# Kernel tuning notes

Hardware: AMD Instinct MI355X
Metric: run time of the kernel (lower is better)

The kernel has to match this reference:

```python
import jax, jax.numpy as jnp
import numpy as np

NUM_GROUPS = 32
EPS = 1e-5

def setup_inputs() -> dict:
    key = jax.random.key(0)
    ks = jax.random.split(key, 10)
    N, C, H, W = 4, 128, 64, 64
    x = jax.random.normal(ks[0], (N, C, H, W), dtype=jnp.float32)
    # GroupNorm affine params
    gn_scale = jnp.ones((C,), dtype=jnp.float32)
    gn_bias = jnp.zeros((C,), dtype=jnp.float32)
    # 1x1 conv weights [out, in] (xavier_uniform scale)
    lim = float(np.sqrt(6.0 / (C + C)))
    wq = jax.random.uniform(ks[1], (C, C), minval=-lim, maxval=lim, dtype=jnp.float32)
    wk = jax.random.uniform(ks[2], (C, C), minval=-lim, maxval=lim, dtype=jnp.float32)
    wv = jax.random.uniform(ks[3], (C, C), minval=-lim, maxval=lim, dtype=jnp.float32)
    wp = jax.random.uniform(ks[4], (C, C), minval=-lim, maxval=lim, dtype=jnp.float32) * 1e-5
    bq = jnp.zeros((C,), dtype=jnp.float32)
    bk = jnp.zeros((C,), dtype=jnp.float32)
    bv = jnp.zeros((C,), dtype=jnp.float32)
    bp = jnp.zeros((C,), dtype=jnp.float32)
    return {"x": x, "gn_scale": gn_scale, "gn_bias": gn_bias,
            "wq": wq, "bq": bq, "wk": wk, "bk": bk,
            "wv": wv, "bv": bv, "wp": wp, "bp": bp}

def _group_norm(x, scale, bias):
    # x: [N, C, H, W]
    N, C, H, W = x.shape
    g = x.reshape(N, NUM_GROUPS, C // NUM_GROUPS, H, W)
    mean = g.mean(axis=(2, 3, 4), keepdims=True)
    var = g.var(axis=(2, 3, 4), keepdims=True)
    g = (g - mean) * jax.lax.rsqrt(var + EPS)
    x = g.reshape(N, C, H, W)
    return x * scale[None, :, None, None] + bias[None, :, None, None]

def reference(x, gn_scale, gn_bias, wq, bq, wk, bk, wv, bv, wp, bp):
    N, C, H, W = x.shape
    h = _group_norm(x, gn_scale, gn_bias)
    # flatten spatial to tokens: [N, HW, C]
    ht = h.reshape(N, C, H * W).transpose(0, 2, 1)
    q = jnp.einsum('nlc,oc->nlo', ht, wq) + bq
    k = jnp.einsum('nlc,oc->nlo', ht, wk) + bk
    v = jnp.einsum('nlc,oc->nlo', ht, wv) + bv
    score = jnp.einsum('nqc,nkc->nqk', q, k) * (C ** -0.5)  # [N, HW, HW]
    attn = jax.nn.softmax(score, axis=-1)
    out = jnp.einsum('nqk,nkc->nqc', attn, v)  # [N, HW, C]
    out = jnp.einsum('nlc,oc->nlo', out, wp) + bp
    out = out.transpose(0, 2, 1).reshape(N, C, H, W)
    return x + out
```

## Files before the change

kernel.cpp:

```cpp
#include <hip/hip_runtime.h>

#define HW 4096
#define CCH 128
#define NB 4

typedef short bf16x8 __attribute__((ext_vector_type(8)));
typedef float f32x4 __attribute__((ext_vector_type(4)));

__device__ __forceinline__ unsigned short f2bf(float f){
  union { float fv; unsigned u; } v; v.fv = f;
  unsigned r = v.u + 0x7fffu + ((v.u >> 16) & 1u);
  return (unsigned short)(r >> 16);
}
__device__ __forceinline__ float bf2f(unsigned short u){
  return __uint_as_float(((unsigned)u) << 16);
}
__device__ __forceinline__ f32x4 mfma16(bf16x8 a, bf16x8 b, f32x4 c){
  return __builtin_amdgcn_mfma_f32_16x16x32_bf16(a, b, c, 0, 0, 0);
}
__device__ __forceinline__ void gll16(const void* g, void* l){
  __builtin_amdgcn_global_load_lds(
      (const __attribute__((address_space(1))) unsigned*)g,
      (__attribute__((address_space(3))) unsigned*)l, 16, 0, 0);
}

__global__ __launch_bounds__(256) void gn_stats_k(const float* __restrict__ x,
    float* __restrict__ stats,
    const float* __restrict__ wq, const float* __restrict__ wk,
    const float* __restrict__ wv, const float* __restrict__ wp,
    unsigned short* __restrict__ wqb, unsigned short* __restrict__ wkb,
    unsigned short* __restrict__ wvb, unsigned short* __restrict__ wpb){
  int tid = threadIdx.x;
  if (tid < 128){
    int f4 = blockIdx.x * 128 + tid;
    int m = f4 >> 12, e = f4 & 4095;
    const float* s4 = (m == 0) ? wq : ((m == 1) ? wk : ((m == 2) ? wv : wp));
    unsigned short* d4 = (m == 0) ? wqb : ((m == 1) ? wkb : ((m == 2) ? wvb : wpb));
    float4 v = *(const float4*)(s4 + e * 4);
    ushort4 b; b.x = f2bf(v.x); b.y = f2bf(v.y); b.z = f2bf(v.z); b.w = f2bf(v.w);
    *(ushort4*)(d4 + e * 4) = b;
  }
  int gid = blockIdx.x;
  const float4* p = (const float4*)(x + (size_t)gid * 16384);
  float s = 0.f, q = 0.f;
  #pragma unroll
  for (int i = 0; i < 16; i++){
    float4 v = p[tid + 256 * i];
    s += v.x + v.y + v.z + v.w;
    q += v.x * v.x + v.y * v.y + v.z * v.z + v.w * v.w;
  }
  #pragma unroll
  for (int d = 1; d < 64; d <<= 1){ s += __shfl_xor(s, d); q += __shfl_xor(q, d); }
  __shared__ float red[8];
  int w = tid >> 6;
  if ((tid & 63) == 0){ red[2 * w] = s; red[2 * w + 1] = q; }
  __syncthreads();
  if (tid == 0){
    float S = red[0] + red[2] + red[4] + red[6];
    float Q = red[1] + red[3] + red[5] + red[7];
    float mean = S * (1.f / 16384.f);
    float var  = Q * (1.f / 16384.f) - mean * mean;
    stats[2 * gid]     = mean;
    stats[2 * gid + 1] = rsqrtf(var + 1e-5f);
  }
}

__global__ __launch_bounds__(256) void gn_apply_k(const float* __restrict__ x,
    const float* __restrict__ stats, const float* __restrict__ sc,
    const float* __restrict__ bi, unsigned short* __restrict__ ht){
  int n = blockIdx.y, l0 = blockIdx.x * 32, tid = threadIdx.x;
  __shared__ __align__(16) unsigned short hs[32][136];
  #pragma unroll
  for (int i = 0; i < 16; i++){
    int c = (tid >> 5) + 8 * i;
    int l = tid & 31;
    float v = x[((size_t)(n * CCH + c)) * HW + l0 + l];
    int grp = n * 32 + (c >> 2);
    float r = (v - stats[2 * grp]) * stats[2 * grp + 1] * sc[c] + bi[c];
    hs[l][c] = f2bf(r);
  }
  __syncthreads();
  #pragma unroll
  for (int i = 0; i < 2; i++){
    int ch = tid + 256 * i;
    int l = ch >> 4, cb = (ch & 15) * 8;
    *(uint4*)&ht[((size_t)(n * HW) + l0 + l) * CCH + cb] = *(const uint4*)&hs[l][cb];
  }
}

__global__ __launch_bounds__(256, 3) void qkv_k(const unsigned short* __restrict__ ht,
    const unsigned short* __restrict__ wqb, const unsigned short* __restrict__ wkb,
    const unsigned short* __restrict__ wvb,
    const float* __restrict__ bq, const float* __restrict__ bk,
    const float* __restrict__ bv,
    unsigned short* __restrict__ Qg, unsigned short* __restrict__ Kg,
    unsigned short* __restrict__ Vt){
  int n = blockIdx.y, l0 = blockIdx.x * 64, m = blockIdx.z, tid = threadIdx.x;
  int w = tid >> 6, lane = tid & 63, l15 = lane & 15, g = lane >> 4;
  __shared__ __align__(16) char lds[49152];
  char* hA = lds;
  char* WB = lds + 16384;
  const unsigned short* wsrc = (m == 0) ? wqb : ((m == 1) ? wkb : wvb);
  const float* bsrc = (m == 0) ? bq : ((m == 1) ? bk : bv);
  {
    const char* hb = (const char*)ht + ((size_t)(n * HW) + l0) * (CCH * 2);
    #pragma unroll
    for (int i = 0; i < 4; i++){
      int T = (4 * w + i) * 64 + lane;
      int row = T >> 4, c16 = (T & 15) ^ (row & 15);
      gll16(hb + row * 256 + c16 * 16, hA + (4 * w + i) * 1024);
    }
    const char* wb2 = (const char*)wsrc;
    #pragma unroll
    for (int i = 0; i < 8; i++){
      int T = (8 * w + i) * 64 + lane;
      int row = T >> 4, c16 = (T & 15) ^ (row & 15);
      gll16(wb2 + row * 256 + c16 * 16, WB + (8 * w + i) * 1024);
    }
  }
  __syncthreads();
  bf16x8 a[4];
  #pragma unroll
  for (int kc = 0; kc < 4; kc++)
    a[kc] = *(const bf16x8*)(hA + (16 * w + l15) * 256 + ((4 * kc + g) ^ l15) * 16);
  f32x4 acc[8];
  #pragma unroll
  for (int ct = 0; ct < 8; ct++) acc[ct] = (f32x4)(0.f);
  #pragma unroll
  for (int ct = 0; ct < 8; ct++)
    #pragma unroll
    for (int kc = 0; kc < 4; kc++){
      bf16x8 bfr = *(const bf16x8*)(WB + (16 * ct + l15) * 256 + ((4 * kc + g) ^ l15) * 16);
      acc[ct] = mfma16(a[kc], bfr, acc[ct]);
    }
  __syncthreads();
  if (m < 2){
    float qs = (m == 0) ? 0.08838834764831845f : 1.0f;
    unsigned short* dst = (m == 0) ? Qg : Kg;
    unsigned short* os = (unsigned short*)(lds + 16384);
    #pragma unroll
    for (int ct = 0; ct < 8; ct++){
      int o = 16 * ct + l15;
      float bias = bsrc[o];
      #pragma unroll
      for (int r = 0; r < 4; r++)
        os[(16 * w + 4 * g + r) * 136 + o] = f2bf((acc[ct][r] + bias) * qs);
    }
    __syncthreads();
    #pragma unroll
    for (int i = 0; i < 4; i++){
      int T = tid + 256 * i;
      int row = T >> 4, cb = T & 15;
      *(uint4*)&dst[((size_t)(n * HW) + l0 + row) * CCH + cb * 8] =
          *(const uint4*)&os[row * 136 + cb * 8];
    }
  } else {
    unsigned short* os = (unsigned short*)(lds + 16384);
    #pragma unroll
    for (int ct = 0; ct < 8; ct++){
      int o = 16 * ct + l15;
      float bias = bsrc[o];
      #pragma unroll
      for (int r = 0; r < 4; r++)
        os[o * 72 + 16 * w + 4 * g + r] = f2bf(acc[ct][r] + bias);
    }
    __syncthreads();
    #pragma unroll
    for (int i = 0; i < 4; i++){
      int T = tid + 256 * i;
      int row = T >> 3, c = T & 7;
      *(uint4*)&Vt[((size_t)(n * CCH) + row) * HW + l0 + c * 8] =
          *(const uint4*)&os[row * 72 + c * 8];
    }
  }
}

__global__ __launch_bounds__(256, 4) void attn_k(const unsigned short* __restrict__ Qg,
    const unsigned short* __restrict__ Kg, const unsigned short* __restrict__ Vt,
    unsigned short* __restrict__ Op, float* __restrict__ Ml, int lsp){
  int nbk = gridDim.x, cpx = nbk >> 3, b = blockIdx.x;
  int swz = (b & 7) * cpx + (b >> 3);
  int q0 = (swz & 63) * 64;
  int rest = swz >> 6;
  int splits = 1 << lsp;
  int sp = rest & (splits - 1);
  int n = rest >> lsp;
  int kvs = HW >> lsp, nt = 64 >> lsp;
  int tid = threadIdx.x;
  int w = tid >> 6, lane = tid & 63, l15 = lane & 15, g = lane >> 4;
  __shared__ __align__(16) char lds[32768];
  char* Ks = lds;
  char* Vs = lds + 16384;

  bf16x8 qf[4];
  #pragma unroll
  for (int kc = 0; kc < 4; kc++)
    qf[kc] = *reinterpret_cast<const bf16x8*>(
        &Qg[((size_t)(n * HW) + q0 + 16 * w + l15) * CCH + 32 * kc + 8 * g]);
  f32x4 ov[8];
  #pragma unroll
  for (int i = 0; i < 8; i++) ov[i] = (f32x4)(0.f);
  float mrun = -3.0e38f, lrun = 0.f;

  const char* kp[4]; const char* vp[4];
  {
    const char* kbase = (const char*)Kg + ((size_t)(n * HW) + sp * kvs) * (CCH * 2);
    const char* vbase = (const char*)Vt + (size_t)(n * CCH) * (HW * 2) + (size_t)sp * kvs * 2;
    #pragma unroll
    for (int i = 0; i < 4; i++){
      int C = (w * 4 + i) * 64 + lane;
      int row = C >> 4, c16 = (C & 15) ^ (row & 15);
      kp[i] = kbase + row * 256 + c16 * 16;
      int vrow = C >> 3, c8 = (C & 7) ^ (vrow & 7);
      vp[i] = vbase + (size_t)vrow * (HW * 2) + c8 * 16;
    }
  }
  char* kl = Ks + w * 4096;
  char* vl = Vs + w * 4096;

  for (int t = 0; t < nt; t++){
    __syncthreads();
    #pragma unroll
    for (int i = 0; i < 4; i++) gll16(kp[i] + (size_t)t * 16384, kl + i * 1024);
    #pragma unroll
    for (int i = 0; i < 4; i++) gll16(vp[i] + (size_t)t * 128,   vl + i * 1024);
    __syncthreads();

    f32x4 s[4];
    __builtin_amdgcn_s_setprio(1);
    #pragma unroll
    for (int ct = 0; ct < 4; ct++){
      f32x4 acc = (f32x4)(0.f);
      #pragma unroll
      for (int kc = 0; kc < 4; kc++){
        bf16x8 kf = *(const bf16x8*)(Ks + (16 * ct + l15) * 256 + ((4 * kc + g) ^ l15) * 16);
        acc = mfma16(kf, qf[kc], acc);
      }
      s[ct] = acc;
    }
    __builtin_amdgcn_s_setprio(0);

    float mx = -3.0e38f;
    #pragma unroll
    for (int ct = 0; ct < 4; ct++)
      #pragma unroll
      for (int r = 0; r < 4; r++) mx = fmaxf(mx, s[ct][r]);
    mx = fmaxf(mx, __shfl_xor(mx, 16));
    mx = fmaxf(mx, __shfl_xor(mx, 32));
    if (__any(mx > mrun + 8.0f)){
      float mn = fmaxf(mrun, mx);
      float al = __expf(mrun - mn);
      mrun = mn; lrun *= al;
      #pragma unroll
      for (int ct = 0; ct < 8; ct++)
        #pragma unroll
        for (int r = 0; r < 4; r++) ov[ct][r] *= al;
    }
    float rs = 0.f;
    #pragma unroll
    for (int ct = 0; ct < 4; ct++)
      #pragma unroll
      for (int r = 0; r < 4; r++){
        float e = __expf(s[ct][r] - mrun);
        s[ct][r] = e;
        rs += e;
      }
    rs += __shfl_xor(rs, 16);
    rs += __shfl_xor(rs, 32);
    lrun += rs;

    unsigned up[4][2];
    #pragma unroll
    for (int ct = 0; ct < 4; ct++)
      #pragma unroll
      for (int h = 0; h < 2; h++)
        up[ct][h] = (unsigned)f2bf(s[ct][2 * h]) |
                    ((unsigned)f2bf(s[ct][2 * h + 1]) << 16);
    union { unsigned u[2][4]; bf16x8 v[2]; } pb;
    #pragma unroll
    for (int kc = 0; kc < 2; kc++)
      #pragma unroll
      for (int j = 0; j < 4; j++){
        int src = (((j + ((g & 1) << 2)) >> 1) << 4) + l15;
        unsigned v0 = (unsigned)__shfl((int)up[2 * kc][j & 1], src);
        unsigned v1 = (unsigned)__shfl((int)up[2 * kc + 1][j & 1], src);
        pb.u[kc][j] = (g & 2) ? v1 : v0;
      }

    __builtin_amdgcn_s_setprio(1);
    #pragma unroll
    for (int ct = 0; ct < 8; ct++){
      #pragma unroll
      for (int kc = 0; kc < 2; kc++){
        bf16x8 vf = *(const bf16x8*)(Vs + (16 * ct + l15) * 128 + ((4 * kc + g) ^ (l15 & 7)) * 16);
        ov[ct] = mfma16(vf, pb.v[kc], ov[ct]);
      }
    }
    __builtin_amdgcn_s_setprio(0);
  }
  float inv = 1.f / lrun;
  (void)inv;
  size_t obase = (size_t)((sp * NB + n) * HW);
  size_t qrow = obase + q0 + 16 * w + l15;
  #pragma unroll
  for (int ct = 0; ct < 8; ct++){
    ushort4 pk;
    pk.x = f2bf(ov[ct][0]); pk.y = f2bf(ov[ct][1]);
    pk.z = f2bf(ov[ct][2]); pk.w = f2bf(ov[ct][3]);
    *(ushort4*)&Op[qrow * CCH + 16 * ct + 4 * g] = pk;
  }
  if (g == 0){
    Ml[qrow * 2]     = mrun;
    Ml[qrow * 2 + 1] = lrun;
  }
}

__global__ __launch_bounds__(256) void projout_k(const unsigned short* __restrict__ Op,
    const float* __restrict__ Ml, const unsigned short* __restrict__ wpb,
    const float* __restrict__ bp, const float* __restrict__ x,
    float* __restrict__ out, int splits){
  int n = blockIdx.y, l0 = blockIdx.x * 32, tid = threadIdx.x;
  int w = tid >> 6, lane = tid & 63, l15 = lane & 15, g = lane >> 4;
  __shared__ __align__(16) unsigned short hs[32][136];
  __shared__ __align__(16) char WB[32768];
  {
    const char* wb2 = (const char*)wpb;
    #pragma unroll
    for (int i = 0; i < 8; i++){
      int T = (8 * w + i) * 64 + lane;
      int row = T >> 4, c16 = (T & 15) ^ (row & 15);
      gll16(wb2 + row * 256 + c16 * 16, WB + (8 * w + i) * 1024);
    }
  }
  const size_t SSTR = (size_t)NB * HW;
  #pragma unroll
  for (int i = 0; i < 2; i++){
    int T = tid + 256 * i;
    int row = T >> 4, cb = (T & 15) * 8;
    size_t gl = (size_t)n * HW + l0 + row;
    float mv = -3.0e38f;
    #pragma unroll
    for (int s = 0; s < 4; s++)
      if (s < splits) mv = fmaxf(mv, Ml[(s * SSTR + gl) * 2]);
    float fa[8];
    #pragma unroll
    for (int j = 0; j < 8; j++) fa[j] = 0.f;
    float denom = 0.f;
    #pragma unroll
    for (int s = 0; s < 4; s++){
      if (s < splits){
        float wgt = __expf(Ml[(s * SSTR + gl) * 2] - mv);
        denom += wgt * Ml[(s * SSTR + gl) * 2 + 1];
        uint4 a = *(const uint4*)&Op[(s * SSTR + gl) * CCH + cb];
        const unsigned short* au = (const unsigned short*)&a;
        #pragma unroll
        for (int j = 0; j < 8; j++) fa[j] += wgt * bf2f(au[j]);
      }
    }
    float inv = 1.f / denom;
    #pragma unroll
    for (int j = 0; j < 8; j++) hs[row][cb + j] = f2bf(fa[j] * inv);
  }
  __syncthreads();
  int rt = w & 1, cg = w >> 1;
  bf16x8 a[4];
  #pragma unroll
  for (int kc = 0; kc < 4; kc++)
    a[kc] = *reinterpret_cast<const bf16x8*>(&hs[16 * rt + l15][32 * kc + 8 * g]);
  f32x4 acc[4];
  #pragma unroll
  for (int ci = 0; ci < 4; ci++) acc[ci] = (f32x4)(0.f);
  #pragma unroll
  for (int ci = 0; ci < 4; ci++){
    int o = 16 * (cg * 4 + ci) + l15;
    #pragma unroll
    for (int kc = 0; kc < 4; kc++){
      bf16x8 bfr = *(const bf16x8*)(WB + o * 256 + ((4 * kc + g) ^ l15) * 16);
      acc[ci] = mfma16(a[kc], bfr, acc[ci]);
    }
  }
  #pragma unroll
  for (int ci = 0; ci < 4; ci++){
    int o = 16 * (cg * 4 + ci) + l15;
    float bias = bp[o];
    size_t base = ((size_t)(n * CCH) + o) * HW + l0 + 16 * rt + 4 * g;
    float4 xr = *(const float4*)&x[base];
    float4 res;
    res.x = xr.x + acc[ci][0] + bias;
    res.y = xr.y + acc[ci][1] + bias;
    res.z = xr.z + acc[ci][2] + bias;
    res.w = xr.w + acc[ci][3] + bias;
    *(float4*)&out[base] = res;
  }
}

extern "C" void kernel_launch(void* const* d_in, const int* in_sizes, int n_in,
                              void* d_out, int out_size, void* d_ws, size_t ws_size,
                              hipStream_t stream){
  const float* x    = (const float*)d_in[0];
  const float* gnsc = (const float*)d_in[1];
  const float* gnb  = (const float*)d_in[2];
  const float* wq   = (const float*)d_in[3];
  const float* bq   = (const float*)d_in[4];
  const float* wk   = (const float*)d_in[5];
  const float* bk   = (const float*)d_in[6];
  const float* wv   = (const float*)d_in[7];
  const float* bv   = (const float*)d_in[8];
  const float* wp   = (const float*)d_in[9];
  const float* bp   = (const float*)d_in[10];
  float* out = (float*)d_out;

  char* ws = (char*)d_ws;
  const size_t BUF = (size_t)NB * HW * CCH * sizeof(unsigned short);
  const size_t WOFF = 4096;
  const size_t HTOFF = WOFF + 4 * 32768;
  const size_t NEED4 = HTOFF + 8 * BUF + (size_t)4 * NB * HW * 2 * sizeof(float);
  const int lsp = (ws_size >= NEED4) ? 2 : 1;
  const int splits = 1 << lsp;

  float* stats        = (float*)ws;
  unsigned short* wqb = (unsigned short*)(ws + WOFF);
  unsigned short* wkb = (unsigned short*)(ws + WOFF + 32768);
  unsigned short* wvb = (unsigned short*)(ws + WOFF + 65536);
  unsigned short* wpb = (unsigned short*)(ws + WOFF + 98304);
  unsigned short* ht  = (unsigned short*)(ws + HTOFF);
  unsigned short* Qg  = (unsigned short*)(ws + HTOFF + BUF);
  unsigned short* Kg  = (unsigned short*)(ws + HTOFF + 2 * BUF);
  unsigned short* Vt  = (unsigned short*)(ws + HTOFF + 3 * BUF);
  unsigned short* Op  = (unsigned short*)(ws + HTOFF + 4 * BUF);
  float*          Ml  = (float*)(ws + HTOFF + 4 * BUF + (size_t)splits * BUF);

  gn_stats_k<<<128, 256, 0, stream>>>(x, stats, wq, wk, wv, wp, wqb, wkb, wvb, wpb);
  gn_apply_k<<<dim3(128, NB), 256, 0, stream>>>(x, stats, gnsc, gnb, ht);
  qkv_k<<<dim3(64, NB, 3), 256, 0, stream>>>(ht, wqb, wkb, wvb, bq, bk, bv, Qg, Kg, Vt);
  attn_k<<<dim3(64 * NB * splits), 256, 0, stream>>>(Qg, Kg, Vt, Op, Ml, lsp);
  projout_k<<<dim3(128, NB), 256, 0, stream>>>(Op, Ml, wpb, bp, x, out, splits);
}
```

Before: 157.6 us.

## Fuse GroupNorm apply into QKV kernel and double-buffer attention KV tiles

The separate GroupNorm-apply kernel is folded into the QKV projection kernel. Each block now normalizes fp32 x directly into a swizzled bf16 LDS tile, which removes the ht intermediate buffer and one kernel launch. The attention kernel switches to 32-key tiles held in two LDS buffers, issuing the next tile's async loads before computing on the current one so memory latency overlaps the MFMA work. The costs are more loop iterations, each with a barrier, smaller MFMA batches per iteration, and a redundant reread of x across the three q/k/v blocks.

Measured after the change: 159.9 us. About the same (+1.4%).

```diff
diff --git a/kernel.cpp b/kernel.cpp
--- a/kernel.cpp
+++ b/kernel.cpp
@@ -65,30 +65,9 @@
   }
 }
 
-__global__ __launch_bounds__(256) void gn_apply_k(const float* __restrict__ x,
+__global__ __launch_bounds__(256, 3) void gnqkv_k(const float* __restrict__ x,
     const float* __restrict__ stats, const float* __restrict__ sc,
-    const float* __restrict__ bi, unsigned short* __restrict__ ht){
-  int n = blockIdx.y, l0 = blockIdx.x * 32, tid = threadIdx.x;
-  __shared__ __align__(16) unsigned short hs[32][136];
-  #pragma unroll
-  for (int i = 0; i < 16; i++){
-    int c = (tid >> 5) + 8 * i;
-    int l = tid & 31;
-    float v = x[((size_t)(n * CCH + c)) * HW + l0 + l];
-    int grp = n * 32 + (c >> 2);
-    float r = (v - stats[2 * grp]) * stats[2 * grp + 1] * sc[c] + bi[c];
-    hs[l][c] = f2bf(r);
-  }
-  __syncthreads();
-  #pragma unroll
-  for (int i = 0; i < 2; i++){
-    int ch = tid + 256 * i;
-    int l = ch >> 4, cb = (ch & 15) * 8;
-    *(uint4*)&ht[((size_t)(n * HW) + l0 + l) * CCH + cb] = *(const uint4*)&hs[l][cb];
-  }
-}
-
-__global__ __launch_bounds__(256, 3) void qkv_k(const unsigned short* __restrict__ ht,
+    const float* __restrict__ bi,
     const unsigned short* __restrict__ wqb, const unsigned short* __restrict__ wkb,
     const unsigned short* __restrict__ wvb,
     const float* __restrict__ bq, const float* __restrict__ bk,
@@ -103,19 +82,33 @@
   const unsigned short* wsrc = (m == 0) ? wqb : ((m == 1) ? wkb : wvb);
   const float* bsrc = (m == 0) ? bq : ((m == 1) ? bk : bv);
   {
-    const char* hb = (const char*)ht + ((size_t)(n * HW) + l0) * (CCH * 2);
-    #pragma unroll
-    for (int i = 0; i < 4; i++){
-      int T = (4 * w + i) * 64 + lane;
-      int row = T >> 4, c16 = (T & 15) ^ (row & 15);
-      gll16(hb + row * 256 + c16 * 16, hA + (4 * w + i) * 1024);
-    }
     const char* wb2 = (const char*)wsrc;
     #pragma unroll
     for (int i = 0; i < 8; i++){
       int T = (8 * w + i) * 64 + lane;
       int row = T >> 4, c16 = (T & 15) ^ (row & 15);
       gll16(wb2 + row * 256 + c16 * 16, WB + (8 * w + i) * 1024);
+    }
+  }
+  #pragma unroll
+  for (int i = 0; i < 8; i++){
+    int F = tid + 256 * i;
+    int c = F >> 4, l4 = F & 15;
+    float4 v = *(const float4*)&x[((size_t)(n * CCH + c)) * HW + l0 + l4 * 4];
+    int grp = n * 32 + (c >> 2);
+    float mean = stats[2 * grp], rstd = stats[2 * grp + 1];
+    float scl = rstd * sc[c];
+    float off = bi[c] - mean * scl;
+    float r0 = v.x * scl + off, r1 = v.y * scl + off;
+    float r2 = v.z * scl + off, r3 = v.w * scl + off;
+    int slotbase = ((c >> 3) << 4) ^ 0;
+    (void)slotbase;
+    #pragma unroll
+    for (int j = 0; j < 4; j++){
+      int l = l4 * 4 + j;
+      float rv = (j == 0) ? r0 : ((j == 1) ? r1 : ((j == 2) ? r2 : r3));
+      int slot = (c >> 3) ^ (l & 15);
+      *(unsigned short*)(hA + l * 256 + slot * 16 + ((c & 7) << 1)) = f2bf(rv);
     }
   }
   __syncthreads();
@@ -185,12 +178,11 @@
   int splits = 1 << lsp;
   int sp = rest & (splits - 1);
   int n = rest >> lsp;
-  int kvs = HW >> lsp, nt = 64 >> lsp;
+  int kvs = HW >> lsp;
+  int nt = kvs >> 5;
   int tid = threadIdx.x;
   int w = tid >> 6, lane = tid & 63, l15 = lane & 15, g = lane >> 4;
   __shared__ __align__(16) char lds[32768];
-  char* Ks = lds;
-  char* Vs = lds + 16384;
 
   bf16x8 qf[4];
   #pragma unroll
@@ -202,49 +194,55 @@
   for (int i = 0; i < 8; i++) ov[i] = (f32x4)(0.f);
   float mrun = -3.0e38f, lrun = 0.f;
 
-  const char* kp[4]; const char* vp[4];
+  const char* kp[2]; const char* vp[2];
   {
     const char* kbase = (const char*)Kg + ((size_t)(n * HW) + sp * kvs) * (CCH * 2);
     const char* vbase = (const char*)Vt + (size_t)(n * CCH) * (HW * 2) + (size_t)sp * kvs * 2;
     #pragma unroll
-    for (int i = 0; i < 4; i++){
-      int C = (w * 4 + i) * 64 + lane;
-      int row = C >> 4, c16 = (C & 15) ^ (row & 15);
-      kp[i] = kbase + row * 256 + c16 * 16;
-      int vrow = C >> 3, c8 = (C & 7) ^ (vrow & 7);
-      vp[i] = vbase + (size_t)vrow * (HW * 2) + c8 * 16;
-    }
-  }
-  char* kl = Ks + w * 4096;
-  char* vl = Vs + w * 4096;
+    for (int i = 0; i < 2; i++){
+      int C = (w * 2 + i) * 64 + lane;
+      int kr = C >> 4, ks = (C & 15) ^ (kr & 15);
+      kp[i] = kbase + kr * 256 + ks * 16;
+      int vr = C >> 2, vsl = (C & 3) ^ ((vr >> 1) & 3);
+      vp[i] = vbase + (size_t)vr * (HW * 2) + vsl * 16;
+    }
+  }
+
+  #pragma unroll
+  for (int i = 0; i < 2; i++){
+    gll16(kp[i], lds + w * 2048 + i * 1024);
+    gll16(vp[i], lds + 8192 + w * 2048 + i * 1024);
+  }
+  __syncthreads();
 
   for (int t = 0; t < nt; t++){
-    __syncthreads();
-    #pragma unroll
-    for (int i = 0; i < 4; i++) gll16(kp[i] + (size_t)t * 16384, kl + i * 1024);
-    #pragma unroll
-    for (int i = 0; i < 4; i++) gll16(vp[i] + (size_t)t * 128,   vl + i * 1024);
-    __syncthreads();
-
-    f32x4 s[4];
+    char* cur = lds + ((t & 1) << 14);
+    if (t + 1 < nt){
+      char* nb = lds + (((t + 1) & 1) << 14);
+      #pragma unroll
+      for (int i = 0; i < 2; i++){
+        gll16(kp[i] + (size_t)(t + 1) * 8192, nb + w * 2048 + i * 1024);
+        gll16(vp[i] + (size_t)(t + 1) * 64,   nb + 8192 + w * 2048 + i * 1024);
+      }
+    }
+    char* Ks = cur; char* Vs = cur + 8192;
+
+    f32x4 s[2];
     __builtin_amdgcn_s_setprio(1);
     #pragma unroll
-    for (int ct = 0; ct < 4; ct++){
+    for (int ct = 0; ct < 2; ct++){
       f32x4 acc = (f32x4)(0.f);
       #pragma unroll
       for (int kc = 0; kc < 4; kc++){
-        bf16x8 kf = *(const bf16x8*)(Ks + (16 * ct + l15) * 256 + ((4 * kc + g) ^ l15) * 16);
+        bf16x8 kf = *(const bf16x8*)(Ks + (16 * ct + l15) * 256 + (((4 * kc + g) ^ l15) << 4));
         acc = mfma16(kf, qf[kc], acc);
       }
       s[ct] = acc;
     }
     __builtin_amdgcn_s_setprio(0);
 
-    float mx = -3.0e38f;
-    #pragma unroll
-    for (int ct = 0; ct < 4; ct++)
-      #pragma unroll
-      for (int r = 0; r < 4; r++) mx = fmaxf(mx, s[ct][r]);
+    float mx = fmaxf(fmaxf(fmaxf(s[0][0], s[0][1]), fmaxf(s[0][2], s[0][3])),
+                     fmaxf(fmaxf(s[1][0], s[1][1]), fmaxf(s[1][2], s[1][3])));
     mx = fmaxf(mx, __shfl_xor(mx, 16));
     mx = fmaxf(mx, __shfl_xor(mx, 32));
     if (__any(mx > mrun + 8.0f)){
@@ -258,7 +256,7 @@
     }
     float rs = 0.f;
     #pragma unroll
-    for (int ct = 0; ct < 4; ct++)
+    for (int ct = 0; ct < 2; ct++)
       #pragma unroll
       for (int r = 0; r < 4; r++){
         float e = __expf(s[ct][r] - mrun);
@@ -269,37 +267,32 @@
     rs += __shfl_xor(rs, 32);
     lrun += rs;
 
-    unsigned up[4][2];
-    #pragma unroll
-    for (int ct = 0; ct < 4; ct++)
+    unsigned up[2][2];
+    #pragma unroll
+    for (int ct = 0; ct < 2; ct++)
       #pragma unroll
       for (int h = 0; h < 2; h++)
         up[ct][h] = (unsigned)f2bf(s[ct][2 * h]) |
                     ((unsigned)f2bf(s[ct][2 * h + 1]) << 16);
-    union { unsigned u[2][4]; bf16x8 v[2]; } pb;
-    #pragma unroll
-    for (int kc = 0; kc < 2; kc++)
-      #pragma unroll
-      for (int j = 0; j < 4; j++){
-        int src = (((j + ((g & 1) << 2)) >> 1) << 4) + l15;
-        unsigned v0 = (unsigned)__shfl((int)up[2 * kc][j & 1], src);
-        unsigned v1 = (unsigned)__shfl((int)up[2 * kc + 1][j & 1], src);
-        pb.u[kc][j] = (g & 2) ? v1 : v0;
-      }
+    union { unsigned u[4]; bf16x8 v; } pb;
+    #pragma unroll
+    for (int j = 0; j < 4; j++){
+      int src = (((((g & 1) << 2) + j) >> 1) << 4) + l15;
+      unsigned v0 = (unsigned)__shfl((int)up[0][j & 1], src);
+      unsigned v1 = (unsigned)__shfl((int)up[1][j & 1], src);
+      pb.u[j] = (g & 2) ? v1 : v0;
+    }
 
     __builtin_amdgcn_s_setprio(1);
     #pragma unroll
     for (int ct = 0; ct < 8; ct++){
-      #pragma unroll
-      for (int kc = 0; kc < 2; kc++){
-        bf16x8 vf = *(const bf16x8*)(Vs + (16 * ct + l15) * 128 + ((4 * kc + g) ^ (l15 & 7)) * 16);
-        ov[ct] = mfma16(vf, pb.v[kc], ov[ct]);
-      }
+      int row = 16 * ct + l15;
+      bf16x8 vf = *(const bf16x8*)(Vs + row * 64 + ((g ^ ((row >> 1) & 3)) << 4));
+      ov[ct] = mfma16(vf, pb.v, ov[ct]);
     }
     __builtin_amdgcn_s_setprio(0);
-  }
-  float inv = 1.f / lrun;
-  (void)inv;
+    __syncthreads();
+  }
   size_t obase = (size_t)((sp * NB + n) * HW);
   size_t qrow = obase + q0 + 16 * w + l15;
   #pragma unroll
@@ -413,8 +406,8 @@
   char* ws = (char*)d_ws;
   const size_t BUF = (size_t)NB * HW * CCH * sizeof(unsigned short);
   const size_t WOFF = 4096;
-  const size_t HTOFF = WOFF + 4 * 32768;
-  const size_t NEED4 = HTOFF + 8 * BUF + (size_t)4 * NB * HW * 2 * sizeof(float);
+  const size_t QOFF = WOFF + 4 * 32768;
+  const size_t NEED4 = QOFF + 7 * BUF + (size_t)4 * NB * HW * 2 * sizeof(float);
   const int lsp = (ws_size >= NEED4) ? 2 : 1;
   const int splits = 1 << lsp;
 
@@ -423,16 +416,15 @@
   unsigned short* wkb = (unsigned short*)(ws + WOFF + 32768);
   unsigned short* wvb = (unsigned short*)(ws + WOFF + 65536);
   unsigned short* wpb = (unsigned short*)(ws + WOFF + 98304);
-  unsigned short* ht  = (unsigned short*)(ws + HTOFF);
-  unsigned short* Qg  = (unsigned short*)(ws + HTOFF + BUF);
-  unsigned short* Kg  = (unsigned short*)(ws + HTOFF + 2 * BUF);
-  unsigned short* Vt  = (unsigned short*)(ws + HTOFF + 3 * BUF);
-  unsigned short* Op  = (unsigned short*)(ws + HTOFF + 4 * BUF);
-  float*          Ml  = (float*)(ws + HTOFF + 4 * BUF + (size_t)splits * BUF);
+  unsigned short* Qg  = (unsigned short*)(ws + QOFF);
+  unsigned short* Kg  = (unsigned short*)(ws + QOFF + BUF);
+  unsigned short* Vt  = (unsigned short*)(ws + QOFF + 2 * BUF);
+  unsigned short* Op  = (unsigned short*)(ws + QOFF + 3 * BUF);
+  float*          Ml  = (float*)(ws + QOFF + 3 * BUF + (size_t)splits * BUF);
 
   gn_stats_k<<<128, 256, 0, stream>>>(x, stats, wq, wk, wv, wp, wqb, wkb, wvb, wpb);
-  gn_apply_k<<<dim3(128, NB), 256, 0, stream>>>(x, stats, gnsc, gnb, ht);
-  qkv_k<<<dim3(64, NB, 3), 256, 0, stream>>>(ht, wqb, wkb, wvb, bq, bk, bv, Qg, Kg, Vt);
+  gnqkv_k<<<dim3(64, NB, 3), 256, 0, stream>>>(x, stats, gnsc, gnb,
+      wqb, wkb, wvb, bq, bk, bv, Qg, Kg, Vt);
   attn_k<<<dim3(64 * NB * splits), 256, 0, stream>>>(Qg, Kg, Vt, Op, Ml, lsp);
   projout_k<<<dim3(128, NB), 256, 0, stream>>>(Op, Ml, wpb, bp, x, out, splits);
 }
```

## Fuse GroupNorm apply into QKV projection and use exp2 softmax with more splits

Applied to the files above, without the earlier changes.

Removes the separate gn_apply kernel and its bf16 ht buffer. Each QKV block now normalizes its own x tile and writes it in swizzled form into LDS. The log2(e) factor is folded into the Q scale so that attention and the split combine use exp2f instead of __expf. It also allows up to 8 KV splits when the workspace is large enough and raises attn occupancy to 5 blocks. In exchange, x is re-read and re-normalized three times, once per Q/K/V block, and the 8-way split adds more partial-output traffic in the combine step.

New measurement: 174.2 us. +10.5%, slower.

```diff
diff --git a/kernel.cpp b/kernel.cpp
--- a/kernel.cpp
+++ b/kernel.cpp
@@ -65,30 +65,9 @@
   }
 }
 
-__global__ __launch_bounds__(256) void gn_apply_k(const float* __restrict__ x,
+__global__ __launch_bounds__(256, 3) void gnqkv_k(const float* __restrict__ x,
     const float* __restrict__ stats, const float* __restrict__ sc,
-    const float* __restrict__ bi, unsigned short* __restrict__ ht){
-  int n = blockIdx.y, l0 = blockIdx.x * 32, tid = threadIdx.x;
-  __shared__ __align__(16) unsigned short hs[32][136];
-  #pragma unroll
-  for (int i = 0; i < 16; i++){
-    int c = (tid >> 5) + 8 * i;
-    int l = tid & 31;
-    float v = x[((size_t)(n * CCH + c)) * HW + l0 + l];
-    int grp = n * 32 + (c >> 2);
-    float r = (v - stats[2 * grp]) * stats[2 * grp + 1] * sc[c] + bi[c];
-    hs[l][c] = f2bf(r);
-  }
-  __syncthreads();
-  #pragma unroll
-  for (int i = 0; i < 2; i++){
-    int ch = tid + 256 * i;
-    int l = ch >> 4, cb = (ch & 15) * 8;
-    *(uint4*)&ht[((size_t)(n * HW) + l0 + l) * CCH + cb] = *(const uint4*)&hs[l][cb];
-  }
-}
-
-__global__ __launch_bounds__(256, 3) void qkv_k(const unsigned short* __restrict__ ht,
+    const float* __restrict__ bi,
     const unsigned short* __restrict__ wqb, const unsigned short* __restrict__ wkb,
     const unsigned short* __restrict__ wvb,
     const float* __restrict__ bq, const float* __restrict__ bk,
@@ -103,13 +82,6 @@
   const unsigned short* wsrc = (m == 0) ? wqb : ((m == 1) ? wkb : wvb);
   const float* bsrc = (m == 0) ? bq : ((m == 1) ? bk : bv);
   {
-    const char* hb = (const char*)ht + ((size_t)(n * HW) + l0) * (CCH * 2);
-    #pragma unroll
-    for (int i = 0; i < 4; i++){
-      int T = (4 * w + i) * 64 + lane;
-      int row = T >> 4, c16 = (T & 15) ^ (row & 15);
-      gll16(hb + row * 256 + c16 * 16, hA + (4 * w + i) * 1024);
-    }
     const char* wb2 = (const char*)wsrc;
     #pragma unroll
     for (int i = 0; i < 8; i++){
@@ -118,6 +90,25 @@
       gll16(wb2 + row * 256 + c16 * 16, WB + (8 * w + i) * 1024);
     }
   }
+  #pragma unroll
+  for (int i = 0; i < 8; i++){
+    int F = tid + 256 * i;
+    int c = F >> 4, l4 = F & 15;
+    float4 v = *(const float4*)&x[((size_t)(n * CCH + c)) * HW + l0 + l4 * 4];
+    int grp = n * 32 + (c >> 2);
+    float mean = stats[2 * grp], rstd = stats[2 * grp + 1];
+    float scl = rstd * sc[c];
+    float off = bi[c] - mean * scl;
+    float r0 = v.x * scl + off, r1 = v.y * scl + off;
+    float r2 = v.z * scl + off, r3 = v.w * scl + off;
+    #pragma unroll
+    for (int j = 0; j < 4; j++){
+      int l = l4 * 4 + j;
+      float rv = (j == 0) ? r0 : ((j == 1) ? r1 : ((j == 2) ? r2 : r3));
+      int slot = (c >> 3) ^ (l & 15);
+      *(unsigned short*)(hA + l * 256 + slot * 16 + ((c & 7) << 1)) = f2bf(rv);
+    }
+  }
   __syncthreads();
   bf16x8 a[4];
   #pragma unroll
@@ -135,7 +126,7 @@
     }
   __syncthreads();
   if (m < 2){
-    float qs = (m == 0) ? 0.08838834764831845f : 1.0f;
+    float qs = (m == 0) ? (0.08838834764831845f * 1.4426950408889634f) : 1.0f;
     unsigned short* dst = (m == 0) ? Qg : Kg;
     unsigned short* os = (unsigned short*)(lds + 16384);
     #pragma unroll
@@ -175,7 +166,7 @@
   }
 }
 
-__global__ __launch_bounds__(256, 4) void attn_k(const unsigned short* __restrict__ Qg,
+__global__ __launch_bounds__(256, 5) void attn_k(const unsigned short* __restrict__ Qg,
     const unsigned short* __restrict__ Kg, const unsigned short* __restrict__ Vt,
     unsigned short* __restrict__ Op, float* __restrict__ Ml, int lsp){
   int nbk = gridDim.x, cpx = nbk >> 3, b = blockIdx.x;
@@ -191,6 +182,7 @@
   __shared__ __align__(16) char lds[32768];
   char* Ks = lds;
   char* Vs = lds + 16384;
+  const float THR = 8.0f * 1.4426950408889634f;
 
   bf16x8 qf[4];
   #pragma unroll
@@ -233,7 +225,7 @@
       f32x4 acc = (f32x4)(0.f);
       #pragma unroll
       for (int kc = 0; kc < 4; kc++){
-        bf16x8 kf = *(const bf16x8*)(Ks + (16 * ct + l15) * 256 + ((4 * kc + g) ^ l15) * 16);
+        bf16x8 kf = *(const bf16x8*)(Ks + (16 * ct + l15) * 256 + (((4 * kc + g) ^ l15) << 4));
         acc = mfma16(kf, qf[kc], acc);
       }
       s[ct] = acc;
@@ -247,9 +239,9 @@
       for (int r = 0; r < 4; r++) mx = fmaxf(mx, s[ct][r]);
     mx = fmaxf(mx, __shfl_xor(mx, 16));
     mx = fmaxf(mx, __shfl_xor(mx, 32));
-    if (__any(mx > mrun + 8.0f)){
+    if (__any(mx > mrun + THR)){
       float mn = fmaxf(mrun, mx);
-      float al = __expf(mrun - mn);
+      float al = exp2f(mrun - mn);
       mrun = mn; lrun *= al;
       #pragma unroll
       for (int ct = 0; ct < 8; ct++)
@@ -261,7 +253,7 @@
     for (int ct = 0; ct < 4; ct++)
       #pragma unroll
       for (int r = 0; r < 4; r++){
-        float e = __expf(s[ct][r] - mrun);
+        float e = exp2f(s[ct][r] - mrun);
         s[ct][r] = e;
         rs += e;
       }
@@ -292,14 +284,12 @@
     for (int ct = 0; ct < 8; ct++){
       #pragma unroll
       for (int kc = 0; kc < 2; kc++){
-        bf16x8 vf = *(const bf16x8*)(Vs + (16 * ct + l15) * 128 + ((4 * kc + g) ^ (l15 & 7)) * 16);
+        bf16x8 vf = *(const bf16x8*)(Vs + (16 * ct + l15) * 128 + (((4 * kc + g) ^ (l15 & 7)) << 4));
         ov[ct] = mfma16(vf, pb.v[kc], ov[ct]);
       }
     }
     __builtin_amdgcn_s_setprio(0);
   }
-  float inv = 1.f / lrun;
-  (void)inv;
   size_t obase = (size_t)((sp * NB + n) * HW);
   size_t qrow = obase + q0 + 16 * w + l15;
   #pragma unroll
@@ -340,16 +330,16 @@
     size_t gl = (size_t)n * HW + l0 + row;
     float mv = -3.0e38f;
     #pragma unroll
-    for (int s = 0; s < 4; s++)
+    for (int s = 0; s < 8; s++)
       if (s < splits) mv = fmaxf(mv, Ml[(s * SSTR + gl) * 2]);
     float fa[8];
     #pragma unroll
     for (int j = 0; j < 8; j++) fa[j] = 0.f;
     float denom = 0.f;
     #pragma unroll
-    for (int s = 0; s < 4; s++){
+    for (int s = 0; s < 8; s++){
       if (s < splits){
-        float wgt = __expf(Ml[(s * SSTR + gl) * 2] - mv);
+        float wgt = exp2f(Ml[(s * SSTR + gl) * 2] - mv);
         denom += wgt * Ml[(s * SSTR + gl) * 2 + 1];
         uint4 a = *(const uint4*)&Op[(s * SSTR + gl) * CCH + cb];
         const unsigned short* au = (const unsigned short*)&a;
@@ -413,9 +403,11 @@
   char* ws = (char*)d_ws;
   const size_t BUF = (size_t)NB * HW * CCH * sizeof(unsigned short);
   const size_t WOFF = 4096;
-  const size_t HTOFF = WOFF + 4 * 32768;
-  const size_t NEED4 = HTOFF + 8 * BUF + (size_t)4 * NB * HW * 2 * sizeof(float);
-  const int lsp = (ws_size >= NEED4) ? 2 : 1;
+  const size_t QOFF = WOFF + 4 * 32768;
+  const size_t MLSZ = (size_t)8 * NB * HW * 2 * sizeof(float);
+  const size_t NEED8 = QOFF + 3 * BUF + 8 * BUF + MLSZ;
+  const size_t NEED4 = QOFF + 3 * BUF + 4 * BUF + MLSZ;
+  const int lsp = (ws_size >= NEED8) ? 3 : ((ws_size >= NEED4) ? 2 : 1);
   const int splits = 1 << lsp;
 
   float* stats        = (float*)ws;
@@ -423,16 +415,15 @@
   unsigned short* wkb = (unsigned short*)(ws + WOFF + 32768);
   unsigned short* wvb = (unsigned short*)(ws + WOFF + 65536);
   unsigned short* wpb = (unsigned short*)(ws + WOFF + 98304);
-  unsigned short* ht  = (unsigned short*)(ws + HTOFF);
-  unsigned short* Qg  = (unsigned short*)(ws + HTOFF + BUF);
-  unsigned short* Kg  = (unsigned short*)(ws + HTOFF + 2 * BUF);
-  unsigned short* Vt  = (unsigned short*)(ws + HTOFF + 3 * BUF);
-  unsigned short* Op  = (unsigned short*)(ws + HTOFF + 4 * BUF);
-  float*          Ml  = (float*)(ws + HTOFF + 4 * BUF + (size_t)splits * BUF);
+  unsigned short* Qg  = (unsigned short*)(ws + QOFF);
+  unsigned short* Kg  = (unsigned short*)(ws + QOFF + BUF);
+  unsigned short* Vt  = (unsigned short*)(ws + QOFF + 2 * BUF);
+  unsigned short* Op  = (unsigned short*)(ws + QOFF + 3 * BUF);
+  float*          Ml  = (float*)(ws + QOFF + 3 * BUF + (size_t)splits * BUF);
 
   gn_stats_k<<<128, 256, 0, stream>>>(x, stats, wq, wk, wv, wp, wqb, wkb, wvb, wpb);
-  gn_apply_k<<<dim3(128, NB), 256, 0, stream>>>(x, stats, gnsc, gnb, ht);
-  qkv_k<<<dim3(64, NB, 3), 256, 0, stream>>>(ht, wqb, wkb, wvb, bq, bk, bv, Qg, Kg, Vt);
+  gnqkv_k<<<dim3(64, NB, 3), 256, 0, stream>>>(x, stats, gnsc, gnb,
+      wqb, wkb, wvb, bq, bk, bv, Qg, Kg, Vt);
   attn_k<<<dim3(64 * NB * splits), 256, 0, stream>>>(Qg, Kg, Vt, Op, Ml, lsp);
   projout_k<<<dim3(128, NB), 256, 0, stream>>>(Op, Ml, wpb, bp, x, out, splits);
 }
```
